# Performance work log

Measured on AMD Instinct MI355X. Metric: run time of the kernel, lower is better.

Reference implementation:

```python
import jax, jax.numpy as jnp
import numpy as np
import math

DIM = 4096
N_HEADS = 32
N_KV_HEADS = 8
HEAD_DIM = DIM // N_HEADS  # 128
N_REP = N_HEADS // N_KV_HEADS  # 4
BATCH = 1
SEQ = 2048
ROPE_THETA = 10000.0


def setup_inputs() -> dict:
    key = jax.random.key(0)
    ks = jax.random.split(key, 6)
    x = jax.random.normal(ks[0], (BATCH, SEQ, DIM), dtype=jnp.float32)
    # torch nn.Linear weights are [out_features, in_features]
    s = 1.0 / math.sqrt(DIM)
    wq = jax.random.normal(ks[1], (N_HEADS * HEAD_DIM, DIM), dtype=jnp.float32) * s
    wk = jax.random.normal(ks[2], (N_KV_HEADS * HEAD_DIM, DIM), dtype=jnp.float32) * s
    wv = jax.random.normal(ks[3], (N_KV_HEADS * HEAD_DIM, DIM), dtype=jnp.float32) * s
    wo = jax.random.normal(ks[4], (DIM, N_HEADS * HEAD_DIM), dtype=jnp.float32) * s
    # precomputed rotary frequencies (real/imag parts of freqs_cis)
    inv_freq = 1.0 / (ROPE_THETA ** (jnp.arange(0, HEAD_DIM, 2, dtype=jnp.float32) / HEAD_DIM))
    t = jnp.arange(SEQ, dtype=jnp.float32)
    freqs = jnp.outer(t, inv_freq)  # [S, HEAD_DIM//2]
    return {"x": x, "wq": wq, "wk": wk, "wv": wv, "wo": wo,
            "freqs_cos": jnp.cos(freqs), "freqs_sin": jnp.sin(freqs)}


def _apply_rotary(t, cos, sin):
    # t: [B, S, H, HD]; cos/sin: [S, HD//2]
    B, S, H, HD = t.shape
    tr = t.reshape(B, S, H, HD // 2, 2)
    re, im = tr[..., 0], tr[..., 1]
    c = cos[None, :, None, :]
    s = sin[None, :, None, :]
    out_re = re * c - im * s
    out_im = re * s + im * c
    return jnp.stack([out_re, out_im], axis=-1).reshape(B, S, H, HD)


def reference(x, wq, wk, wv, wo, freqs_cos, freqs_sin):
    B, S, _ = x.shape
    q = jnp.einsum('bsd,od->bso', x, wq).reshape(B, S, N_HEADS, HEAD_DIM)
    k = jnp.einsum('bsd,od->bso', x, wk).reshape(B, S, N_KV_HEADS, HEAD_DIM)
    v = jnp.einsum('bsd,od->bso', x, wv).reshape(B, S, N_KV_HEADS, HEAD_DIM)
    q = _apply_rotary(q, freqs_cos, freqs_sin)
    k = _apply_rotary(k, freqs_cos, freqs_sin)
    # repeat kv heads (GQA): [B,S,Hkv,HD] -> [B,S,H,HD]
    k = jnp.repeat(k, N_REP, axis=2)
    v = jnp.repeat(v, N_REP, axis=2)
    # SDPA with causal mask
    scale = 1.0 / math.sqrt(HEAD_DIM)
    scores = jnp.einsum('bqhd,bkhd->bhqk', q, k) * scale
    causal = jnp.tril(jnp.ones((S, S), dtype=bool))
    scores = jnp.where(causal[None, None], scores, jnp.finfo(scores.dtype).min)
    attn = jax.nn.softmax(scores, axis=-1)
    y = jnp.einsum('bhqk,bkhd->bqhd', attn, v).reshape(B, S, N_HEADS * HEAD_DIM)
    return jnp.einsum('bso,do->bsd', y, wo)
```

## Files before the change

kernel.cpp:

```cpp
#include <hip/hip_runtime.h>
#include <hip/hip_bf16.h>
#include <stdint.h>

typedef unsigned short u16;
typedef __bf16 bf16_8 __attribute__((ext_vector_type(8)));
typedef float f32x4 __attribute__((ext_vector_type(4)));

#define SEQ 2048
#define DIM 4096
#define NH 32
#define NKV 8
#define HD 128
#define QSCALE_LOG2E 0.12753785222167917f

__device__ inline u16 f2bf(float f) {
    unsigned int u = __float_as_uint(f);
    unsigned int r = (u + 0x7fffu + ((u >> 16) & 1u)) >> 16;
    return (u16)r;
}

__device__ inline void async16(const void* g, void* l) {
    __builtin_amdgcn_global_load_lds(
        (const __attribute__((address_space(1))) void*)g,
        (__attribute__((address_space(3))) void*)l, 16, 0, 0);
}

__global__ __launch_bounds__(256) void cast_all(const float* __restrict__ x,
                                                const float* __restrict__ wq,
                                                const float* __restrict__ wk,
                                                const float* __restrict__ wv,
                                                const float* __restrict__ wo,
                                                u16* __restrict__ dst) {
    size_t i4 = (size_t)blockIdx.x * 256 + threadIdx.x;
    size_t e = i4 * 4;
    const float* src;
    size_t off;
    if (e < 8388608ull)       { src = x;  off = 0; }
    else if (e < 25165824ull) { src = wq; off = 8388608ull; }
    else if (e < 29360128ull) { src = wk; off = 25165824ull; }
    else if (e < 33554432ull) { src = wv; off = 29360128ull; }
    else                      { src = wo; off = 33554432ull; }
    float4 v = ((const float4*)src)[i4 - off / 4];
    ushort4 o;
    o.x = f2bf(v.x); o.y = f2bf(v.y); o.z = f2bf(v.z); o.w = f2bf(v.w);
    ((ushort4*)dst)[i4] = o;
}

template <int MODE>
__global__ __launch_bounds__(512, 2) void gemm8p(const u16* __restrict__ A,
                                                 const u16* __restrict__ B,
                                                 void* __restrict__ C0,
                                                 void* __restrict__ C1,
                                                 void* __restrict__ C2,
                                                 const float* __restrict__ fc,
                                                 const float* __restrict__ fs,
                                                 int M, int N, int K) {
    extern __shared__ u16 sm[];
    u16* As = sm;
    u16* Bs = sm + 2 * 256 * 64;

    const int tid = threadIdx.x;
    const int lane = tid & 63;
    const int wid = tid >> 6;
    const int wr = wid >> 2;
    const int wc = wid & 3;
    const int quad = lane >> 4;
    const int l16 = lane & 15;

    const int nwg = gridDim.x * gridDim.y;
    int id = blockIdx.y * gridDim.x + blockIdx.x;
    int swz = (id & 7) * (nwg >> 3) + (id >> 3);
    const int bm = (swz / gridDim.x) * 256;
    const int bn = (swz % gridDim.x) * 256;

    f32x4 acc[8][4] = {};

    auto stageB = [&](int t, int h) {
        const int k0 = t << 6;
        const int buf = t & 1;
#pragma unroll
        for (int r = 0; r < 2; ++r) {
            int S = r * 512 + tid;
            int row = h * 128 + (S >> 3);
            int ch = (S & 7) ^ (row & 7);
            const u16* g = &B[(size_t)(bn + row) * K + k0 + ch * 8];
            async16(g, (void*)&Bs[buf * 16384 + row * 64 + (S & 7) * 8]);
        }
    };
    auto stageA = [&](int t, int qq) {
        const int k0 = t << 6;
        const int buf = t & 1;
#pragma unroll
        for (int r = 0; r < 2; ++r) {
            int row = r * 128 + qq * 64 + (tid >> 3);
            int ch = (tid & 7) ^ (row & 7);
            const u16* g = &A[(size_t)(bm + row) * K + k0 + ch * 8];
            async16(g, (void*)&As[buf * 16384 + row * 64 + (tid & 7) * 8]);
        }
    };

    const int chsw = l16 & 7;
    bf16_8 bfr[4][2];

#define PHASE(qq, STAGE_STMT, VM_STMT)                                          \
    {                                                                           \
        STAGE_STMT;                                                             \
        VM_STMT;                                                                \
        asm volatile("s_barrier" ::: "memory");                                 \
        if (qq == 0) {                                                          \
            _Pragma("unroll")                                                   \
            for (int j = 0; j < 4; ++j)                                         \
                _Pragma("unroll")                                               \
                for (int kk = 0; kk < 2; ++kk)                                  \
                    bfr[j][kk] = *(const bf16_8*)&bs[(j * 16 + l16) * 64 +      \
                                                     (((kk * 4 + quad) ^ chsw) << 3)]; \
        }                                                                       \
        bf16_8 afr[2][2];                                                       \
        _Pragma("unroll")                                                       \
        for (int i = 0; i < 2; ++i)                                             \
            _Pragma("unroll")                                                   \
            for (int kk = 0; kk < 2; ++kk)                                      \
                afr[i][kk] = *(const bf16_8*)&as[((qq * 2 + i) * 16 + l16) * 64 + \
                                                 (((kk * 4 + quad) ^ chsw) << 3)]; \
        __builtin_amdgcn_s_setprio(1);                                          \
        _Pragma("unroll")                                                       \
        for (int kk = 0; kk < 2; ++kk)                                          \
            _Pragma("unroll")                                                   \
            for (int i = 0; i < 2; ++i)                                         \
                _Pragma("unroll")                                               \
                for (int j = 0; j < 4; ++j)                                     \
                    acc[qq * 2 + i][j] = __builtin_amdgcn_mfma_f32_16x16x32_bf16( \
                        afr[i][kk], bfr[j][kk], acc[qq * 2 + i][j], 0, 0, 0);   \
        __builtin_amdgcn_s_setprio(0);                                          \
    }

    const int NT = K >> 6;

    stageB(0, 0); stageB(0, 1); stageA(0, 0); stageA(0, 1);

    for (int t = 0; t < NT - 1; ++t) {
        const int buf = t & 1;
        const u16* as = As + buf * 16384 + wr * (128 * 64);
        const u16* bs = Bs + buf * 16384 + wc * (64 * 64);
        PHASE(0, stageB(t + 1, 0), asm volatile("s_waitcnt vmcnt(4)" ::: "memory"))
        PHASE(1, stageB(t + 1, 1), )
        PHASE(2, stageA(t + 1, 0), asm volatile("s_waitcnt vmcnt(6)" ::: "memory"))
        PHASE(3, stageA(t + 1, 1), )
    }
    {
        const int buf = (NT - 1) & 1;
        const u16* as = As + buf * 16384 + wr * (128 * 64);
        const u16* bs = Bs + buf * 16384 + wc * (64 * 64);
        PHASE(0, , asm volatile("s_waitcnt vmcnt(2)" ::: "memory"))
        PHASE(1, , )
        PHASE(2, , asm volatile("s_waitcnt vmcnt(0)" ::: "memory"))
        PHASE(3, , )
    }
#undef PHASE

    const int wm = wr * 128;
    const int wn = wc * 64;

    if (MODE == 0) {
        float* Cf = (float*)C0;
#pragma unroll
        for (int i = 0; i < 8; ++i)
#pragma unroll
            for (int j = 0; j < 4; ++j)
#pragma unroll
                for (int r = 0; r < 4; ++r)
                    Cf[(size_t)(bm + wm + i * 16 + quad * 4 + r) * N + (bn + wn + j * 16 + l16)] =
                        acc[i][j][r];
    } else {
        u16* Qb = (u16*)C0;
        u16* Kb = (u16*)C1;
        u16* Vt = (u16*)C2;
        if (bn < 5120) {
            const bool isQ = bn < 4096;
            const float osc = isQ ? QSCALE_LOG2E : 1.0f;
#pragma unroll
            for (int i = 0; i < 8; ++i)
#pragma unroll
                for (int j = 0; j < 4; ++j) {
                    int n = bn + wn + j * 16 + l16;
                    int pp = (n & 127) >> 1;
                    bool odd = (l16 & 1);
#pragma unroll
                    for (int r = 0; r < 4; ++r) {
                        int m = bm + wm + i * 16 + quad * 4 + r;
                        float v = acc[i][j][r];
                        float u = __shfl_xor(v, 1);
                        float c = fc[m * 64 + pp];
                        float s = fs[m * 64 + pp];
                        float o = (odd ? (u * s + v * c) : (v * c - u * s)) * osc;
                        if (isQ)
                            Qb[(size_t)m * 4096 + n] = f2bf(o);
                        else
                            Kb[(size_t)m * 1024 + (n - 4096)] = f2bf(o);
                    }
                }
        } else {
#pragma unroll
            for (int i = 0; i < 8; ++i)
#pragma unroll
                for (int j = 0; j < 4; ++j) {
                    int n = bn + wn + j * 16 + l16;
                    ushort4 o;
                    o.x = f2bf(acc[i][j][0]);
                    o.y = f2bf(acc[i][j][1]);
                    o.z = f2bf(acc[i][j][2]);
                    o.w = f2bf(acc[i][j][3]);
                    *(ushort4*)&Vt[(size_t)(n - 5120) * SEQ + (bm + wm + i * 16 + quad * 4)] = o;
                }
        }
    }
}

__global__ __launch_bounds__(256, 4) void attn_k(const u16* __restrict__ Q,
                                                 const u16* __restrict__ Kb,
                                                 const u16* __restrict__ Vt,
                                                 u16* __restrict__ Y) {
    __shared__ u16 Ks[64 * 128];
    __shared__ u16 Vs[128 * 64];
    __shared__ u16 Ps[4 * 16 * 64];
    const int tid = threadIdx.x;
    const int lane = tid & 63;
    const int w = tid >> 6;
    const int quad = lane >> 4;
    const int l16 = lane & 15;
    const int id = blockIdx.x;
    const int qt = 31 - (id >> 5);
    const int h = id & 31;
    const int kvh = h >> 2;
    const size_t qrow0 = (size_t)qt * 64;

    bf16_8 qf[4];
#pragma unroll
    for (int ks = 0; ks < 4; ++ks)
        qf[ks] = *(const bf16_8*)&Q[(qrow0 + w * 16 + l16) * DIM + h * HD + ks * 32 + quad * 8];

    f32x4 po[8] = {};
    float lsum = 0.f;

    char* psbase = (char*)Ps + w * 2048 + l16 * 128;
    const int sw = (l16 & 7) << 1;

    for (int kt = 0; kt <= qt; ++kt) {
#pragma unroll
        for (int r = 0; r < 4; ++r) {
            int S = r * 256 + tid;
            {
                int row = S >> 4, slot = S & 15;
                int chunk = slot ^ (row & 15);
                const char* g = (const char*)Kb +
                    (((size_t)kt * 64 + row) * 1024 + kvh * HD + chunk * 8) * 2;
                async16(g, (char*)Ks + S * 16);
            }
            {
                int row = S >> 3, slot = S & 7;
                int chunk = slot ^ (row & 7);
                const char* g = (const char*)Vt +
                    (((size_t)(kvh * HD + row)) * SEQ + kt * 64 + chunk * 8) * 2;
                async16(g, (char*)Vs + S * 16);
            }
        }
        __syncthreads();

        f32x4 sc[4] = {};
#pragma unroll
        for (int ks = 0; ks < 4; ++ks)
#pragma unroll
            for (int jb = 0; jb < 4; ++jb) {
                bf16_8 kb = *(const bf16_8*)&Ks[(jb * 16 + l16) * 128 + ((ks * 4 + quad) ^ l16) * 8];
                sc[jb] = __builtin_amdgcn_mfma_f32_16x16x32_bf16(kb, qf[ks], sc[jb], 0, 0, 0);
            }

        float pv[4][4];
#pragma unroll
        for (int jb = 0; jb < 4; ++jb)
#pragma unroll
            for (int r = 0; r < 4; ++r)
                pv[jb][r] = exp2f(sc[jb][r]);

        if (kt == qt) {
            int qloc = w * 16 + l16;
#pragma unroll
            for (int jb = 0; jb < 4; ++jb)
#pragma unroll
                for (int r = 0; r < 4; ++r)
                    if (jb * 16 + quad * 4 + r > qloc) pv[jb][r] = 0.f;
        }

#pragma unroll
        for (int jb = 0; jb < 4; ++jb) {
            lsum += (pv[jb][0] + pv[jb][1]) + (pv[jb][2] + pv[jb][3]);
            ushort4 pk;
            pk.x = f2bf(pv[jb][0]);
            pk.y = f2bf(pv[jb][1]);
            pk.z = f2bf(pv[jb][2]);
            pk.w = f2bf(pv[jb][3]);
            int c = jb * 4 + quad;
            *(ushort4*)(psbase + ((c ^ sw) << 3)) = pk;
        }

#pragma unroll
        for (int ks = 0; ks < 2; ++ks) {
            int c = ks * 8 + quad * 2;
            bf16_8 pf = *(const bf16_8*)(psbase + ((c ^ sw) << 3));
#pragma unroll
            for (int n = 0; n < 8; ++n) {
                bf16_8 vf = *(const bf16_8*)&Vs[(n * 16 + l16) * 64 + (((ks * 4 + quad) ^ (l16 & 7))) * 8];
                po[n] = __builtin_amdgcn_mfma_f32_16x16x32_bf16(pf, vf, po[n], 0, 0, 0);
            }
        }
        __syncthreads();
    }

    lsum += __shfl_xor(lsum, 16);
    lsum += __shfl_xor(lsum, 32);
    float inv = 1.f / lsum;
#pragma unroll
    for (int r = 0; r < 4; ++r) {
        float invr = __shfl(inv, quad * 4 + r);
        size_t row = qrow0 + w * 16 + quad * 4 + r;
#pragma unroll
        for (int n = 0; n < 8; ++n)
            Y[row * DIM + h * HD + n * 16 + l16] = f2bf(po[n][r] * invr);
    }
}

extern "C" void kernel_launch(void* const* d_in, const int* in_sizes, int n_in,
                              void* d_out, int out_size, void* d_ws, size_t ws_size,
                              hipStream_t stream) {
    const float* x  = (const float*)d_in[0];
    const float* wq = (const float*)d_in[1];
    const float* wk = (const float*)d_in[2];
    const float* wv = (const float*)d_in[3];
    const float* wo = (const float*)d_in[4];
    const float* fc = (const float*)d_in[5];
    const float* fs = (const float*)d_in[6];

    char* ws = (char*)d_ws;
    const size_t MB = 1u << 20;
    u16* xb    = (u16*)(ws);
    u16* wqkvb = (u16*)(ws + 16 * MB);
    u16* wob   = (u16*)(ws + 64 * MB);
    u16* Qb    = (u16*)(ws + 96 * MB);
    u16* Kb    = (u16*)(ws + 112 * MB);
    u16* Vtb   = (u16*)(ws + 116 * MB);
    u16* Yb    = (u16*)(ws + 120 * MB);

    const int smbytes = 4 * 256 * 64 * 2;
    static int inited = 0;
    if (!inited) {
        hipFuncSetAttribute(reinterpret_cast<const void*>(&gemm8p<1>),
                            hipFuncAttributeMaxDynamicSharedMemorySize, smbytes);
        hipFuncSetAttribute(reinterpret_cast<const void*>(&gemm8p<0>),
                            hipFuncAttributeMaxDynamicSharedMemorySize, smbytes);
        inited = 1;
    }

    cast_all<<<49152, 256, 0, stream>>>(x, wq, wk, wv, wo, (u16*)ws);

    gemm8p<1><<<dim3(24, 8), 512, smbytes, stream>>>(xb, wqkvb, Qb, Kb, Vtb, fc, fs,
                                                     2048, 6144, 4096);

    attn_k<<<dim3(1024), 256, 0, stream>>>(Qb, Kb, Vtb, Yb);

    gemm8p<0><<<dim3(16, 8), 512, smbytes, stream>>>(Yb, wob, (float*)d_out, nullptr, nullptr,
                                                     nullptr, nullptr, 2048, 4096, 4096);
}
```

Baseline: 507.0 us.

## Restructure GEMM pipeline with per-wave staging and smaller output-projection tiles

Reworks the GEMM main loop so each wave stages its own slice of the A/B tiles, LDS fragment reads are issued before the async global loads, and a barrier follows each MFMA phase. The output-projection GEMM moves to a 256x128 tile with a 32x8 grid (256 workgroups instead of 128) so it fills more CUs, and its LDS footprint shrinks. The aim is better overlap of loads with MFMA and higher occupancy for the final GEMM. The cost is an extra barrier per phase and more, smaller workgroups.

New measurement: 514.8 us. Within noise of the previous version (+1.5%).

```diff
diff --git a/kernel.cpp b/kernel.cpp
--- a/kernel.cpp
+++ b/kernel.cpp
@@ -55,116 +55,133 @@
                                                  const float* __restrict__ fc,
                                                  const float* __restrict__ fs,
                                                  int M, int N, int K) {
+    constexpr int BM = 256;
+    constexpr int BN = (MODE == 1) ? 256 : 128;
+    constexpr int WCN = (MODE == 1) ? 4 : 2;
+    constexpr int WM = (MODE == 1) ? 128 : 64;
+    constexpr int AI = WM / 16;
+    constexpr int PAI = AI / 4;
+    constexpr int NBU = (MODE == 1) ? 2 : 1;
+    constexpr int NU = NBU + 2;
+
     extern __shared__ u16 sm[];
     u16* As = sm;
-    u16* Bs = sm + 2 * 256 * 64;
+    u16* Bs = sm + 2 * BM * 64;
 
     const int tid = threadIdx.x;
     const int lane = tid & 63;
     const int wid = tid >> 6;
-    const int wr = wid >> 2;
-    const int wc = wid & 3;
+    const int wr = wid / WCN;
+    const int wc = wid % WCN;
     const int quad = lane >> 4;
     const int l16 = lane & 15;
+    const int l8hi = lane >> 3;
+    const int l8lo = lane & 7;
 
     const int nwg = gridDim.x * gridDim.y;
     int id = blockIdx.y * gridDim.x + blockIdx.x;
     int swz = (id & 7) * (nwg >> 3) + (id >> 3);
-    const int bm = (swz / gridDim.x) * 256;
-    const int bn = (swz % gridDim.x) * 256;
-
-    f32x4 acc[8][4] = {};
-
-    auto stageB = [&](int t, int h) {
+    const int bm = (swz / gridDim.x) * BM;
+    const int bn = (swz % gridDim.x) * BN;
+
+    f32x4 acc[AI][4] = {};
+
+    auto stage_unit = [&](int t, int u) {
+        const int buf = t & 1;
         const int k0 = t << 6;
-        const int buf = t & 1;
-#pragma unroll
-        for (int r = 0; r < 2; ++r) {
-            int S = r * 512 + tid;
-            int row = h * 128 + (S >> 3);
-            int ch = (S & 7) ^ (row & 7);
-            const u16* g = &B[(size_t)(bn + row) * K + k0 + ch * 8];
-            async16(g, (void*)&Bs[buf * 16384 + row * 64 + (S & 7) * 8]);
-        }
-    };
-    auto stageA = [&](int t, int qq) {
-        const int k0 = t << 6;
-        const int buf = t & 1;
-#pragma unroll
-        for (int r = 0; r < 2; ++r) {
-            int row = r * 128 + qq * 64 + (tid >> 3);
-            int ch = (tid & 7) ^ (row & 7);
-            const u16* g = &A[(size_t)(bm + row) * K + k0 + ch * 8];
-            async16(g, (void*)&As[buf * 16384 + row * 64 + (tid & 7) * 8]);
+        const int ch = l8lo ^ l8hi;
+        if (u < NBU) {
+            int row0 = (MODE == 1) ? (wc * 64 + wr * 32 + u * 16)
+                                   : (wc * 64 + wr * 16);
+#pragma unroll
+            for (int r = 0; r < 2; ++r) {
+                int R = row0 + r * 8;
+                const u16* g = &B[(size_t)(bn + R + l8hi) * K + k0 + ch * 8];
+                async16(g, (void*)&Bs[buf * (BN * 64) + R * 64 + lane * 8]);
+            }
+        } else {
+            int q = u - NBU;
+            int row0 = (MODE == 1) ? (wr * 128 + q * 64 + wc * 16)
+                                   : (wr * 64 + q * 32 + wc * 16);
+#pragma unroll
+            for (int r = 0; r < 2; ++r) {
+                int R = row0 + r * 8;
+                const u16* g = &A[(size_t)(bm + R + l8hi) * K + k0 + ch * 8];
+                async16(g, (void*)&As[buf * (BM * 64) + R * 64 + lane * 8]);
+            }
         }
     };
 
     const int chsw = l16 & 7;
     bf16_8 bfr[4][2];
 
-#define PHASE(qq, STAGE_STMT, VM_STMT)                                          \
-    {                                                                           \
-        STAGE_STMT;                                                             \
-        VM_STMT;                                                                \
-        asm volatile("s_barrier" ::: "memory");                                 \
-        if (qq == 0) {                                                          \
-            _Pragma("unroll")                                                   \
-            for (int j = 0; j < 4; ++j)                                         \
-                _Pragma("unroll")                                               \
-                for (int kk = 0; kk < 2; ++kk)                                  \
-                    bfr[j][kk] = *(const bf16_8*)&bs[(j * 16 + l16) * 64 +      \
+#define PHASE(Q, STAGE_STMT, VM_STMT)                                             \
+    {                                                                             \
+        const int buf = t & 1;                                                    \
+        const u16* as = As + buf * (BM * 64) + wr * (WM * 64);                    \
+        const u16* bs = Bs + buf * (BN * 64) + wc * (64 * 64);                    \
+        if (Q == 0) {                                                             \
+            _Pragma("unroll")                                                     \
+            for (int j = 0; j < 4; ++j)                                           \
+                _Pragma("unroll")                                                 \
+                for (int kk = 0; kk < 2; ++kk)                                    \
+                    bfr[j][kk] = *(const bf16_8*)&bs[(j * 16 + l16) * 64 +        \
                                                      (((kk * 4 + quad) ^ chsw) << 3)]; \
-        }                                                                       \
-        bf16_8 afr[2][2];                                                       \
-        _Pragma("unroll")                                                       \
-        for (int i = 0; i < 2; ++i)                                             \
-            _Pragma("unroll")                                                   \
-            for (int kk = 0; kk < 2; ++kk)                                      \
-                afr[i][kk] = *(const bf16_8*)&as[((qq * 2 + i) * 16 + l16) * 64 + \
+        }                                                                         \
+        bf16_8 afr[PAI][2];                                                       \
+        _Pragma("unroll")                                                         \
+        for (int i = 0; i < PAI; ++i)                                             \
+            _Pragma("unroll")                                                     \
+            for (int kk = 0; kk < 2; ++kk)                                        \
+                afr[i][kk] = *(const bf16_8*)&as[((Q * PAI + i) * 16 + l16) * 64 + \
                                                  (((kk * 4 + quad) ^ chsw) << 3)]; \
-        __builtin_amdgcn_s_setprio(1);                                          \
-        _Pragma("unroll")                                                       \
-        for (int kk = 0; kk < 2; ++kk)                                          \
-            _Pragma("unroll")                                                   \
-            for (int i = 0; i < 2; ++i)                                         \
-                _Pragma("unroll")                                               \
-                for (int j = 0; j < 4; ++j)                                     \
-                    acc[qq * 2 + i][j] = __builtin_amdgcn_mfma_f32_16x16x32_bf16( \
-                        afr[i][kk], bfr[j][kk], acc[qq * 2 + i][j], 0, 0, 0);   \
-        __builtin_amdgcn_s_setprio(0);                                          \
+        STAGE_STMT;                                                               \
+        VM_STMT;                                                                  \
+        asm volatile("s_barrier" ::: "memory");                                   \
+        asm volatile("s_waitcnt lgkmcnt(0)" ::: "memory");                        \
+        __builtin_amdgcn_s_setprio(1);                                            \
+        _Pragma("unroll")                                                         \
+        for (int kk = 0; kk < 2; ++kk)                                            \
+            _Pragma("unroll")                                                     \
+            for (int i = 0; i < PAI; ++i)                                         \
+                _Pragma("unroll")                                                 \
+                for (int j = 0; j < 4; ++j)                                       \
+                    acc[Q * PAI + i][j] = __builtin_amdgcn_mfma_f32_16x16x32_bf16( \
+                        afr[i][kk], bfr[j][kk], acc[Q * PAI + i][j], 0, 0, 0);    \
+        __builtin_amdgcn_s_setprio(0);                                            \
+        asm volatile("s_barrier" ::: "memory");                                   \
     }
 
     const int NT = K >> 6;
 
-    stageB(0, 0); stageB(0, 1); stageA(0, 0); stageA(0, 1);
+#pragma unroll
+    for (int u = 0; u < NU; ++u) stage_unit(0, u);
+    asm volatile("s_waitcnt vmcnt(2)" ::: "memory");
+    asm volatile("s_barrier" ::: "memory");
 
     for (int t = 0; t < NT - 1; ++t) {
-        const int buf = t & 1;
-        const u16* as = As + buf * 16384 + wr * (128 * 64);
-        const u16* bs = Bs + buf * 16384 + wc * (64 * 64);
-        PHASE(0, stageB(t + 1, 0), asm volatile("s_waitcnt vmcnt(4)" ::: "memory"))
-        PHASE(1, stageB(t + 1, 1), )
-        PHASE(2, stageA(t + 1, 0), asm volatile("s_waitcnt vmcnt(6)" ::: "memory"))
-        PHASE(3, stageA(t + 1, 1), )
+        PHASE(0, stage_unit(t + 1, 0), )
+        PHASE(1, stage_unit(t + 1, 1), asm volatile("s_waitcnt vmcnt(4)" ::: "memory"))
+        PHASE(2, stage_unit(t + 1, 2), )
+        PHASE(3, if (NU > 3) stage_unit(t + 1, 3),
+                 asm volatile("s_waitcnt vmcnt(2)" ::: "memory"))
     }
     {
-        const int buf = (NT - 1) & 1;
-        const u16* as = As + buf * 16384 + wr * (128 * 64);
-        const u16* bs = Bs + buf * 16384 + wc * (64 * 64);
-        PHASE(0, , asm volatile("s_waitcnt vmcnt(2)" ::: "memory"))
-        PHASE(1, , )
-        PHASE(2, , asm volatile("s_waitcnt vmcnt(0)" ::: "memory"))
+        const int t = NT - 1;
+        PHASE(0, , )
+        PHASE(1, , asm volatile("s_waitcnt vmcnt(0)" ::: "memory"))
+        PHASE(2, , )
         PHASE(3, , )
     }
 #undef PHASE
 
-    const int wm = wr * 128;
+    const int wm = wr * WM;
     const int wn = wc * 64;
 
     if (MODE == 0) {
         float* Cf = (float*)C0;
 #pragma unroll
-        for (int i = 0; i < 8; ++i)
+        for (int i = 0; i < AI; ++i)
 #pragma unroll
             for (int j = 0; j < 4; ++j)
 #pragma unroll
@@ -179,7 +196,7 @@
             const bool isQ = bn < 4096;
             const float osc = isQ ? QSCALE_LOG2E : 1.0f;
 #pragma unroll
-            for (int i = 0; i < 8; ++i)
+            for (int i = 0; i < AI; ++i)
 #pragma unroll
                 for (int j = 0; j < 4; ++j) {
                     int n = bn + wn + j * 16 + l16;
@@ -201,7 +218,7 @@
                 }
         } else {
 #pragma unroll
-            for (int i = 0; i < 8; ++i)
+            for (int i = 0; i < AI; ++i)
 #pragma unroll
                 for (int j = 0; j < 4; ++j) {
                     int n = bn + wn + j * 16 + l16;
@@ -350,23 +367,24 @@
     u16* Vtb   = (u16*)(ws + 116 * MB);
     u16* Yb    = (u16*)(ws + 120 * MB);
 
-    const int smbytes = 4 * 256 * 64 * 2;
+    const int sm1 = (2 * 256 * 64 + 2 * 256 * 64) * 2;
+    const int sm0 = (2 * 256 * 64 + 2 * 128 * 64) * 2;
     static int inited = 0;
     if (!inited) {
         hipFuncSetAttribute(reinterpret_cast<const void*>(&gemm8p<1>),
-                            hipFuncAttributeMaxDynamicSharedMemorySize, smbytes);
+                            hipFuncAttributeMaxDynamicSharedMemorySize, sm1);
         hipFuncSetAttribute(reinterpret_cast<const void*>(&gemm8p<0>),
-                            hipFuncAttributeMaxDynamicSharedMemorySize, smbytes);
+                            hipFuncAttributeMaxDynamicSharedMemorySize, sm0);
         inited = 1;
     }
 
     cast_all<<<49152, 256, 0, stream>>>(x, wq, wk, wv, wo, (u16*)ws);
 
-    gemm8p<1><<<dim3(24, 8), 512, smbytes, stream>>>(xb, wqkvb, Qb, Kb, Vtb, fc, fs,
-                                                     2048, 6144, 4096);
+    gemm8p<1><<<dim3(24, 8), 512, sm1, stream>>>(xb, wqkvb, Qb, Kb, Vtb, fc, fs,
+                                                 2048, 6144, 4096);
 
     attn_k<<<dim3(1024), 256, 0, stream>>>(Qb, Kb, Vtb, Yb);
 
-    gemm8p<0><<<dim3(16, 8), 512, smbytes, stream>>>(Yb, wob, (float*)d_out, nullptr, nullptr,
-                                                     nullptr, nullptr, 2048, 4096, 4096);
-}
+    gemm8p<0><<<dim3(32, 8), 512, sm0, stream>>>(Yb, wob, (float*)d_out, nullptr, nullptr,
+                                                 nullptr, nullptr, 2048, 4096, 4096);
+}
```

## Deepen GEMM prefetch pipeline and halve output-projection tile height

Applied to the files above, without the earlier changes.

The QKV GEMM now loads LDS fragments before issuing the next global-to-LDS stages and keeps loads two k-steps ahead, with a second barrier per phase, so copies overlap more with MFMA work. The output-projection GEMM switches to 128x256 tiles with a 16x16 grid, which doubles the workgroup count to fill more compute units. It also uses a two-phase schedule that reuses A fragments across B sub-tiles. The extra barriers and finely tuned vmcnt counts add synchronisation cost and the risk of subtle ordering bugs.

New measurement: 477.1 us. 1.06x faster.

```diff
diff --git a/kernel.cpp b/kernel.cpp
--- a/kernel.cpp
+++ b/kernel.cpp
@@ -55,9 +55,14 @@
                                                  const float* __restrict__ fc,
                                                  const float* __restrict__ fs,
                                                  int M, int N, int K) {
+    constexpr int BM = (MODE == 1) ? 256 : 128;
+    constexpr int BN = 256;
+    constexpr int WM = (MODE == 1) ? 128 : 64;
+    constexpr int AI = WM / 16;
+
     extern __shared__ u16 sm[];
     u16* As = sm;
-    u16* Bs = sm + 2 * 256 * 64;
+    u16* Bs = sm + 2 * BM * 64;
 
     const int tid = threadIdx.x;
     const int lane = tid & 63;
@@ -70,101 +75,175 @@
     const int nwg = gridDim.x * gridDim.y;
     int id = blockIdx.y * gridDim.x + blockIdx.x;
     int swz = (id & 7) * (nwg >> 3) + (id >> 3);
-    const int bm = (swz / gridDim.x) * 256;
-    const int bn = (swz % gridDim.x) * 256;
-
-    f32x4 acc[8][4] = {};
-
-    auto stageB = [&](int t, int h) {
+    const int bm = (swz / gridDim.x) * BM;
+    const int bn = (swz % gridDim.x) * BN;
+
+    f32x4 acc[AI][4] = {};
+
+    auto stB = [&](int t, int half) {
+        const int buf = t & 1;
         const int k0 = t << 6;
-        const int buf = t & 1;
 #pragma unroll
         for (int r = 0; r < 2; ++r) {
             int S = r * 512 + tid;
-            int row = h * 128 + (S >> 3);
+            int row = S >> 3;
+            int phys = half * 32 + (row >> 5) * 64 + (row & 31);
             int ch = (S & 7) ^ (row & 7);
-            const u16* g = &B[(size_t)(bn + row) * K + k0 + ch * 8];
-            async16(g, (void*)&Bs[buf * 16384 + row * 64 + (S & 7) * 8]);
+            const u16* g = &B[(size_t)(bn + phys) * K + k0 + ch * 8];
+            async16(g, (void*)&Bs[buf * (256 * 64) + phys * 64 + (S & 7) * 8]);
         }
     };
-    auto stageA = [&](int t, int qq) {
+    auto stA = [&](int t, int half) {
+        const int buf = t & 1;
         const int k0 = t << 6;
+#pragma unroll
+        for (int r = 0; r < 2; ++r) {
+            int S = r * 512 + tid;
+            int row = S >> 3;
+            int phys = half * 64 + (row & 63) + (row >> 6) * 128;
+            int ch = (S & 7) ^ (row & 7);
+            const u16* g = &A[(size_t)(bm + phys) * K + k0 + ch * 8];
+            async16(g, (void*)&As[buf * (BM * 64) + phys * 64 + (S & 7) * 8]);
+        }
+    };
+    auto stA0 = [&](int t) {
         const int buf = t & 1;
+        const int k0 = t << 6;
 #pragma unroll
         for (int r = 0; r < 2; ++r) {
-            int row = r * 128 + qq * 64 + (tid >> 3);
-            int ch = (tid & 7) ^ (row & 7);
+            int S = r * 512 + tid;
+            int row = S >> 3;
+            int ch = (S & 7) ^ (row & 7);
             const u16* g = &A[(size_t)(bm + row) * K + k0 + ch * 8];
-            async16(g, (void*)&As[buf * 16384 + row * 64 + (tid & 7) * 8]);
+            async16(g, (void*)&As[buf * (BM * 64) + row * 64 + (S & 7) * 8]);
         }
     };
 
     const int chsw = l16 & 7;
-    bf16_8 bfr[4][2];
-
-#define PHASE(qq, STAGE_STMT, VM_STMT)                                          \
+    const int NT = K >> 6;
+
+#define VMW(n) asm volatile("s_waitcnt vmcnt(" #n ")" ::: "memory")
+#define BAR() asm volatile("s_barrier" ::: "memory")
+
+    if constexpr (MODE == 1) {
+        bf16_8 bh[4][2];
+
+#define M1PHASE(T, P, STAGE_STMT, VM_STMT)                                      \
     {                                                                           \
+        const u16* as = As + ((T) & 1) * (BM * 64) + wr * (128 * 64);           \
+        const u16* bs = Bs + ((T) & 1) * (256 * 64) + wc * (64 * 64);           \
+        bf16_8 afr[2][2];                                                       \
+        _Pragma("unroll") for (int i = 0; i < 2; ++i)                           \
+        _Pragma("unroll") for (int kk = 0; kk < 2; ++kk)                        \
+            afr[i][kk] = *(const bf16_8*)&as[(((P) * 2 + i) * 16 + l16) * 64 +  \
+                                             (((kk * 4 + quad) ^ chsw) << 3)];  \
+        if ((P) == 0) {                                                         \
+            _Pragma("unroll") for (int j = 0; j < 4; ++j)                       \
+            _Pragma("unroll") for (int kk = 0; kk < 2; ++kk)                    \
+                bh[j][kk] = *(const bf16_8*)&bs[(j * 16 + l16) * 64 +           \
+                                             (((kk * 4 + quad) ^ chsw) << 3)];  \
+        }                                                                       \
         STAGE_STMT;                                                             \
         VM_STMT;                                                                \
-        asm volatile("s_barrier" ::: "memory");                                 \
-        if (qq == 0) {                                                          \
-            _Pragma("unroll")                                                   \
-            for (int j = 0; j < 4; ++j)                                         \
-                _Pragma("unroll")                                               \
-                for (int kk = 0; kk < 2; ++kk)                                  \
-                    bfr[j][kk] = *(const bf16_8*)&bs[(j * 16 + l16) * 64 +      \
-                                                     (((kk * 4 + quad) ^ chsw) << 3)]; \
+        BAR();                                                                  \
+        __builtin_amdgcn_s_setprio(1);                                          \
+        _Pragma("unroll") for (int kk = 0; kk < 2; ++kk)                        \
+        _Pragma("unroll") for (int i = 0; i < 2; ++i)                           \
+        _Pragma("unroll") for (int j = 0; j < 4; ++j)                           \
+            acc[(P) * 2 + i][j] = __builtin_amdgcn_mfma_f32_16x16x32_bf16(      \
+                afr[i][kk], bh[j][kk], acc[(P) * 2 + i][j], 0, 0, 0);           \
+        __builtin_amdgcn_s_setprio(0);                                          \
+        BAR();                                                                  \
+    }
+
+        stB(0, 0); stB(0, 1); stA(0, 0); stA(0, 1);
+        stB(1, 0); stB(1, 1); stA(1, 0);
+        VMW(6);
+        BAR();
+
+        for (int t = 0; t < NT - 2; ++t) {
+            M1PHASE(t, 0, stA(t + 1, 1), )
+            M1PHASE(t, 1, stB(t + 2, 0), VMW(10))
+            M1PHASE(t, 2, stB(t + 2, 1), )
+            M1PHASE(t, 3, stA(t + 2, 0), VMW(8))
+        }
+        {
+            const int t = NT - 2;
+            M1PHASE(t, 0, stA(NT - 1, 1), )
+            M1PHASE(t, 1, , VMW(8))
+            M1PHASE(t, 2, , )
+            M1PHASE(t, 3, , VMW(2))
+        }
+        {
+            const int t = NT - 1;
+            M1PHASE(t, 0, , )
+            M1PHASE(t, 1, , VMW(0))
+            M1PHASE(t, 2, , )
+            M1PHASE(t, 3, , )
+        }
+#undef M1PHASE
+    } else {
+        bf16_8 ah[4][2];
+
+#define M0PHASE(T, P, STAGE_STMT, VM_STMT)                                      \
+    {                                                                           \
+        const u16* as = As + ((T) & 1) * (BM * 64) + wr * (64 * 64);            \
+        const u16* bs = Bs + ((T) & 1) * (256 * 64) + wc * (64 * 64);           \
+        if ((P) == 0) {                                                         \
+            _Pragma("unroll") for (int i = 0; i < 4; ++i)                       \
+            _Pragma("unroll") for (int kk = 0; kk < 2; ++kk)                    \
+                ah[i][kk] = *(const bf16_8*)&as[(i * 16 + l16) * 64 +           \
+                                             (((kk * 4 + quad) ^ chsw) << 3)];  \
         }                                                                       \
-        bf16_8 afr[2][2];                                                       \
-        _Pragma("unroll")                                                       \
-        for (int i = 0; i < 2; ++i)                                             \
-            _Pragma("unroll")                                                   \
-            for (int kk = 0; kk < 2; ++kk)                                      \
-                afr[i][kk] = *(const bf16_8*)&as[((qq * 2 + i) * 16 + l16) * 64 + \
-                                                 (((kk * 4 + quad) ^ chsw) << 3)]; \
+        bf16_8 bfr[2][2];                                                       \
+        _Pragma("unroll") for (int j = 0; j < 2; ++j)                           \
+        _Pragma("unroll") for (int kk = 0; kk < 2; ++kk)                        \
+            bfr[j][kk] = *(const bf16_8*)&bs[(((P) * 2 + j) * 16 + l16) * 64 +  \
+                                             (((kk * 4 + quad) ^ chsw) << 3)];  \
+        STAGE_STMT;                                                             \
+        VM_STMT;                                                                \
+        BAR();                                                                  \
         __builtin_amdgcn_s_setprio(1);                                          \
-        _Pragma("unroll")                                                       \
-        for (int kk = 0; kk < 2; ++kk)                                          \
-            _Pragma("unroll")                                                   \
-            for (int i = 0; i < 2; ++i)                                         \
-                _Pragma("unroll")                                               \
-                for (int j = 0; j < 4; ++j)                                     \
-                    acc[qq * 2 + i][j] = __builtin_amdgcn_mfma_f32_16x16x32_bf16( \
-                        afr[i][kk], bfr[j][kk], acc[qq * 2 + i][j], 0, 0, 0);   \
+        _Pragma("unroll") for (int kk = 0; kk < 2; ++kk)                        \
+        _Pragma("unroll") for (int i = 0; i < 4; ++i)                           \
+        _Pragma("unroll") for (int j = 0; j < 2; ++j)                           \
+            acc[i][(P) * 2 + j] = __builtin_amdgcn_mfma_f32_16x16x32_bf16(      \
+                ah[i][kk], bfr[j][kk], acc[i][(P) * 2 + j], 0, 0, 0);           \
         __builtin_amdgcn_s_setprio(0);                                          \
-    }
-
-    const int NT = K >> 6;
-
-    stageB(0, 0); stageB(0, 1); stageA(0, 0); stageA(0, 1);
-
-    for (int t = 0; t < NT - 1; ++t) {
-        const int buf = t & 1;
-        const u16* as = As + buf * 16384 + wr * (128 * 64);
-        const u16* bs = Bs + buf * 16384 + wc * (64 * 64);
-        PHASE(0, stageB(t + 1, 0), asm volatile("s_waitcnt vmcnt(4)" ::: "memory"))
-        PHASE(1, stageB(t + 1, 1), )
-        PHASE(2, stageA(t + 1, 0), asm volatile("s_waitcnt vmcnt(6)" ::: "memory"))
-        PHASE(3, stageA(t + 1, 1), )
-    }
-    {
-        const int buf = (NT - 1) & 1;
-        const u16* as = As + buf * 16384 + wr * (128 * 64);
-        const u16* bs = Bs + buf * 16384 + wc * (64 * 64);
-        PHASE(0, , asm volatile("s_waitcnt vmcnt(2)" ::: "memory"))
-        PHASE(1, , )
-        PHASE(2, , asm volatile("s_waitcnt vmcnt(0)" ::: "memory"))
-        PHASE(3, , )
-    }
-#undef PHASE
-
-    const int wm = wr * 128;
+        BAR();                                                                  \
+    }
+
+        stA0(0); stB(0, 0); stB(0, 1);
+        stA0(1); stB(1, 0);
+        VMW(4);
+        BAR();
+
+        for (int t = 0; t < NT - 2; ++t) {
+            M0PHASE(t, 0, stB(t + 1, 1), VMW(6))
+            M0PHASE(t, 1, { stA0(t + 2); stB(t + 2, 0); }, VMW(6))
+        }
+        {
+            const int t = NT - 2;
+            M0PHASE(t, 0, stB(NT - 1, 1), VMW(6))
+            M0PHASE(t, 1, , VMW(2))
+        }
+        {
+            const int t = NT - 1;
+            M0PHASE(t, 0, , VMW(0))
+            M0PHASE(t, 1, , )
+        }
+#undef M0PHASE
+    }
+#undef VMW
+#undef BAR
+
+    const int wm = wr * WM;
     const int wn = wc * 64;
 
     if (MODE == 0) {
         float* Cf = (float*)C0;
 #pragma unroll
-        for (int i = 0; i < 8; ++i)
+        for (int i = 0; i < AI; ++i)
 #pragma unroll
             for (int j = 0; j < 4; ++j)
 #pragma unroll
@@ -179,7 +258,7 @@
             const bool isQ = bn < 4096;
             const float osc = isQ ? QSCALE_LOG2E : 1.0f;
 #pragma unroll
-            for (int i = 0; i < 8; ++i)
+            for (int i = 0; i < AI; ++i)
 #pragma unroll
                 for (int j = 0; j < 4; ++j) {
                     int n = bn + wn + j * 16 + l16;
@@ -201,7 +280,7 @@
                 }
         } else {
 #pragma unroll
-            for (int i = 0; i < 8; ++i)
+            for (int i = 0; i < AI; ++i)
 #pragma unroll
                 for (int j = 0; j < 4; ++j) {
                     int n = bn + wn + j * 16 + l16;
@@ -350,23 +429,24 @@
     u16* Vtb   = (u16*)(ws + 116 * MB);
     u16* Yb    = (u16*)(ws + 120 * MB);
 
-    const int smbytes = 4 * 256 * 64 * 2;
+    const int sm1 = (2 * 256 * 64 + 2 * 256 * 64) * 2;
+    const int sm0 = (2 * 128 * 64 + 2 * 256 * 64) * 2;
     static int inited = 0;
     if (!inited) {
         hipFuncSetAttribute(reinterpret_cast<const void*>(&gemm8p<1>),
-                            hipFuncAttributeMaxDynamicSharedMemorySize, smbytes);
+                            hipFuncAttributeMaxDynamicSharedMemorySize, sm1);
         hipFuncSetAttribute(reinterpret_cast<const void*>(&gemm8p<0>),
-                            hipFuncAttributeMaxDynamicSharedMemorySize, smbytes);
+                            hipFuncAttributeMaxDynamicSharedMemorySize, sm0);
         inited = 1;
     }
 
     cast_all<<<49152, 256, 0, stream>>>(x, wq, wk, wv, wo, (u16*)ws);
 
-    gemm8p<1><<<dim3(24, 8), 512, smbytes, stream>>>(xb, wqkvb, Qb, Kb, Vtb, fc, fs,
-                                                     2048, 6144, 4096);
+    gemm8p<1><<<dim3(24, 8), 512, sm1, stream>>>(xb, wqkvb, Qb, Kb, Vtb, fc, fs,
+                                                 2048, 6144, 4096);
 
     attn_k<<<dim3(1024), 256, 0, stream>>>(Qb, Kb, Vtb, Yb);
 
-    gemm8p<0><<<dim3(16, 8), 512, smbytes, stream>>>(Yb, wob, (float*)d_out, nullptr, nullptr,
-                                                     nullptr, nullptr, 2048, 4096, 4096);
-}
+    gemm8p<0><<<dim3(16, 16), 512, sm0, stream>>>(Yb, wob, (float*)d_out, nullptr, nullptr,
+                                                  nullptr, nullptr, 2048, 4096, 4096);
+}
```
